# Optimization experiments

Measured on AMD Instinct MI355X. Metric: run time of the kernel, lower is better.

The kernel has to match this reference:

```python
import jax, jax.numpy as jnp
import numpy as np

P = 16384        # nodes per detector layer
NLAYERS = 5      # conf.nlayers (layer labels 0..NLAYERS)
NPROP = 1        # conf.model.nprop
D, S, H = 64, 16, 256   # dyn_features, static_features, deeplayer_nodes
E = 262144       # edges per edge-set (avg degree 16)
NG = 64          # num_graphs


def setup_inputs() -> dict:
    key = jax.random.key(0)
    ks = jax.random.split(key, 20)
    N = P * (NLAYERS + 1)
    F = D + S
    sc = 0.05
    ri = lambda k, shape: jax.random.randint(k, shape, 0, P, dtype=jnp.int32)
    return {
        "x0": jax.random.normal(ks[0], (N, 1), jnp.float32),
        "static": jax.random.normal(ks[1], (N, S), jnp.float32),
        "W1": jax.random.normal(ks[2], (4, F, H), jnp.float32) * sc,
        "b1": jax.random.normal(ks[3], (4, H), jnp.float32) * sc,
        "W2": jax.random.normal(ks[4], (4, H, H), jnp.float32) * sc,
        "b2": jax.random.normal(ks[5], (4, H), jnp.float32) * sc,
        "W3": jax.random.normal(ks[6], (4, H, D), jnp.float32) * sc,
        "b3": jax.random.normal(ks[7], (4, D), jnp.float32) * sc,
        "eps": jnp.zeros((3,), jnp.float32),
        "lin_w": jax.random.normal(ks[8], (D, 1), jnp.float32) * sc,
        "lin_b": jax.random.normal(ks[9], (1,), jnp.float32) * sc,
        "inner_src": ri(ks[10], (NLAYERS, E)),
        "inner_dst": ri(ks[11], (NLAYERS, E)),
        "fwd_src": ri(ks[12], (NLAYERS - 1, E)),
        "fwd_dst": ri(ks[13], (NLAYERS - 1, E)),
        "bwd_src": ri(ks[14], (NLAYERS - 1, E)),
        "bwd_dst": ri(ks[15], (NLAYERS - 1, E)),
        "batch_idx": jax.random.randint(ks[16], (N,), 0, NG, dtype=jnp.int32),
        "num_graphs": NG,
    }


def reference(x0, static, W1, b1, W2, b2, W3, b3, eps, lin_w, lin_b,
              inner_src, inner_dst, fwd_src, fwd_dst, bwd_src, bwd_dst,
              batch_idx, num_graphs):
    N = x0.shape[0]

    def mlp(i, h):
        # dnn(): Linear(F,H)+ReLU, Linear(H,H)+ReLU, Linear(H,D)+ReLU
        h = jax.nn.relu(h @ W1[i] + b1[i])
        h = jax.nn.relu(h @ W2[i] + b2[i])
        return jax.nn.relu(h @ W3[i] + b3[i])

    def gin(i, xs, src, dst):
        # GINConv(train_eps=True): mlp((1+eps)*x + sum_{j in N(v)} x_j)
        aggr = jax.ops.segment_sum(xs[src], dst, num_segments=xs.shape[0])
        return mlp(i, (1.0 + eps[i]) * xs + aggr)

    # x = hstack(batch.x, zeros(N, D-1))
    x = jnp.concatenate([x0, jnp.zeros((N, D - 1), x0.dtype)], axis=1)

    for _ in range(NPROP):
        for il in range(NLAYERS):
            s0 = il * P
            # inner conv on layer il (addstatic over that layer's nodes)
            xs = jnp.concatenate([x[s0:s0 + P], static[s0:s0 + P]], axis=1)
            x = x.at[s0:s0 + P].set(gin(0, xs, inner_src[il], inner_dst[il]))
            if il == NLAYERS - 1:
                continue
            # forward conv over layers il (local [0,P)) and il+1 (local [P,2P))
            xs2 = jnp.concatenate([x[s0:s0 + 2 * P], static[s0:s0 + 2 * P]], axis=1)
            out = gin(1, xs2, fwd_src[il], fwd_dst[il] + P)
            x = x.at[s0 + P:s0 + 2 * P].set(out[P:])
            # node_dnn on target layer
            xt = jnp.concatenate([x[s0 + P:s0 + 2 * P], static[s0 + P:s0 + 2 * P]], axis=1)
            x = x.at[s0 + P:s0 + 2 * P].set(mlp(3, xt))
        for il in range(NLAYERS - 1, 0, -1):
            s0 = (il - 1) * P
            # backward conv: layer il (local [P,2P)) -> layer il-1 (local [0,P))
            xs2 = jnp.concatenate([x[s0:s0 + 2 * P], static[s0:s0 + 2 * P]], axis=1)
            out = gin(2, xs2, bwd_src[il - 1] + P, bwd_dst[il - 1])
            x = x.at[s0:s0 + P].set(out[:P])
            # inner conv on layer il-1
            xs = jnp.concatenate([x[s0:s0 + P], static[s0:s0 + P]], axis=1)
            x = x.at[s0:s0 + P].set(gin(0, xs, inner_src[il - 1], inner_dst[il - 1]))
            # node_dnn on layer il-1
            xt = jnp.concatenate([x[s0:s0 + P], static[s0:s0 + P]], axis=1)
            x = x.at[s0:s0 + P].set(mlp(3, xt))

    pooled = jax.ops.segment_sum(x, batch_idx, num_segments=num_graphs)
    return jax.nn.relu(pooled @ lin_w + lin_b)
```

## Files before the change

kernel.cpp:

```cpp
#include <hip/hip_runtime.h>

#define P 16384
#define NLAYERS 5
#define NND 98304
#define D 64
#define S 16
#define F 80
#define KP1 96
#define H 256
#define EDG 262144
#define NG 64
#define NSETS 13
#define RSP 16385
#define LDP 40
#define LH2 264
#define LXS 100

typedef __attribute__((ext_vector_type(8))) _Float16 f16x8;
typedef __attribute__((ext_vector_type(4))) _Float16 f16x4;
typedef __attribute__((ext_vector_type(4))) float f32x4;

__device__ __forceinline__ void fatomic_add(float* p, float v) {
    unsafeAtomicAdd(p, v);
}

__global__ void k_init_x(const float* __restrict__ x0, float* __restrict__ X,
                         _Float16* __restrict__ Xh,
                         int* __restrict__ deg, float* __restrict__ PL) {
    int idx = blockIdx.x * blockDim.x + threadIdx.x;
    if (idx < NND * D) {
        int row = idx >> 6, f = idx & 63;
        float v = (f == 0) ? x0[row] : 0.0f;
        X[idx] = v;
        Xh[idx] = (_Float16)v;
        return;
    }
    int r = idx - NND * D;
    if (r < NSETS * P) { deg[r] = 0; return; }
    r -= NSETS * P;
    if (r < NG * D) PL[r] = 0.0f;
}

__global__ void k_wconv_all(const float* __restrict__ W1, const float* __restrict__ W2,
                            const float* __restrict__ W3, const float* __restrict__ stat,
                            _Float16* __restrict__ w1, _Float16* __restrict__ w2,
                            _Float16* __restrict__ w3, _Float16* __restrict__ st16) {
    const int n1 = 4 * H * KP1, n2 = 4 * H * H, n3 = 4 * D * H;
    int idx = blockIdx.x * blockDim.x + threadIdx.x;
    if (idx >= n1 + n2 + n3) {
        int i = idx - (n1 + n2 + n3);
        if (i < NND * S) st16[i] = (_Float16)stat[i];
        return;
    }
    const float* W; _Float16* h; int K, N, Kp, i;
    if (idx < n1)              { W = W1; h = w1; K = F; N = H; Kp = KP1; i = idx; }
    else if (idx < n1 + n2)    { W = W2; h = w2; K = H; N = H; Kp = H;   i = idx - n1; }
    else                       { W = W3; h = w3; K = H; N = D; Kp = H;  i = idx - n1 - n2; }
    int set = i / (N * Kp), rem = i - set * (N * Kp);
    int n = rem / Kp, kp = rem - n * Kp;
    float v = (kp < K) ? W[(size_t)set * K * N + (size_t)kp * N + n] : 0.0f;
    h[i] = (_Float16)v;
}

__device__ __forceinline__ const int* set_ptr(int t, const int* inner, const int* fwd,
                                              const int* bwd) {
    if (t < 5) return inner + (size_t)t * EDG;
    if (t < 9) return fwd + (size_t)(t - 5) * EDG;
    return bwd + (size_t)(t - 9) * EDG;
}

__global__ void k_csr_hist(const int* __restrict__ inner_dst, const int* __restrict__ fwd_dst,
                           const int* __restrict__ bwd_dst, int* __restrict__ deg,
                           int* __restrict__ rank) {
    int idx = blockIdx.x * blockDim.x + threadIdx.x;
    if (idx >= NSETS * EDG) return;
    int t = idx >> 18, e = idx & (EDG - 1);
    const int* dstp = set_ptr(t, inner_dst, fwd_dst, bwd_dst);
    rank[idx] = atomicAdd(&deg[t * P + dstp[e]], 1);
}

__global__ __launch_bounds__(1024) void k_csr_scan(const int* __restrict__ deg,
                                                   int* __restrict__ rowstart) {
    __shared__ int part[1024];
    int t = blockIdx.x;
    const int* d = deg + t * P;
    int* rs = rowstart + (size_t)t * RSP;
    int tid = threadIdx.x;
    int base = tid * 16;
    int loc[16], sum = 0;
#pragma unroll
    for (int i = 0; i < 16; ++i) { loc[i] = sum; sum += d[base + i]; }
    part[tid] = sum;
    __syncthreads();
    for (int off = 1; off < 1024; off <<= 1) {
        int v = (tid >= off) ? part[tid - off] : 0;
        __syncthreads();
        part[tid] += v;
        __syncthreads();
    }
    int pre = tid ? part[tid - 1] : 0;
#pragma unroll
    for (int i = 0; i < 16; ++i) rs[base + i] = pre + loc[i];
    if (tid == 1023) rs[P] = pre + sum;
}

__global__ void k_csr_scatter(const int* __restrict__ inner_src, const int* __restrict__ inner_dst,
                              const int* __restrict__ fwd_src, const int* __restrict__ fwd_dst,
                              const int* __restrict__ bwd_src, const int* __restrict__ bwd_dst,
                              const int* __restrict__ rowstart, const int* __restrict__ rank,
                              int* __restrict__ elist) {
    int idx = blockIdx.x * blockDim.x + threadIdx.x;
    if (idx >= NSETS * EDG) return;
    int t = idx >> 18, e = idx & (EDG - 1);
    const int* srcp = set_ptr(t, inner_src, fwd_src, bwd_src);
    const int* dstp = set_ptr(t, inner_dst, fwd_dst, bwd_dst);
    int dv = dstp[e];
    elist[(size_t)t * EDG + rowstart[(size_t)t * RSP + dv] + rank[idx]] = srcp[e];
}

__global__ __launch_bounds__(256) void k_gather_T(const float* __restrict__ X,
                                                  const _Float16* __restrict__ Xh,
                                                  const _Float16* __restrict__ st16,
                                                  const int* __restrict__ elist,
                                                  const int* __restrict__ rowstart,
                                                  _Float16* __restrict__ Th,
                                                  int dst_gbase, int src_gbase,
                                                  const float* __restrict__ eps, int ei,
                                                  const float* __restrict__ stf) {
    int wv = threadIdx.x >> 6, l = threadIdx.x & 63;
    int v = blockIdx.x * 4 + wv;
    int beg = rowstart[v], end = rowstart[v + 1];
    float scale = 1.0f + eps[ei];
    int rg = l >> 4, c = l & 15;
    float ax0 = 0.f, ax1 = 0.f, ax2 = 0.f, ax3 = 0.f, as = 0.f;
    int i = beg;
    for (; i + 4 <= end; i += 4) {
        int s = src_gbase + elist[i + rg];
        f16x4 xv = *(const f16x4*)&Xh[(size_t)s * D + 4 * c];
        ax0 += (float)xv[0]; ax1 += (float)xv[1]; ax2 += (float)xv[2]; ax3 += (float)xv[3];
        as += (float)st16[(size_t)s * S + c];
    }
    if (i < end) {
        int rem = end - i;
        if (rg < rem) {
            int s = src_gbase + elist[i + rg];
            f16x4 xv = *(const f16x4*)&Xh[(size_t)s * D + 4 * c];
            ax0 += (float)xv[0]; ax1 += (float)xv[1]; ax2 += (float)xv[2]; ax3 += (float)xv[3];
            as += (float)st16[(size_t)s * S + c];
        }
    }
#pragma unroll
    for (int off = 16; off < 64; off <<= 1) {
        ax0 += __shfl_xor(ax0, off, 64);
        ax1 += __shfl_xor(ax1, off, 64);
        ax2 += __shfl_xor(ax2, off, 64);
        ax3 += __shfl_xor(ax3, off, 64);
        as  += __shfl_xor(as,  off, 64);
    }
    if (l < 16) {
        int g = dst_gbase + v;
        float4 sx = *(const float4*)&X[(size_t)g * D + 4 * l];
        f16x4 hv;
        hv[0] = (_Float16)(ax0 + scale * sx.x);
        hv[1] = (_Float16)(ax1 + scale * sx.y);
        hv[2] = (_Float16)(ax2 + scale * sx.z);
        hv[3] = (_Float16)(ax3 + scale * sx.w);
        *(f16x4*)&Th[(size_t)v * KP1 + 4 * l] = hv;
        Th[(size_t)v * KP1 + D + l] = (_Float16)(as + scale * stf[(size_t)g * S + l]);
        Th[(size_t)v * KP1 + F + l] = (_Float16)0.0f;
    }
}

template<int MODE>
__global__ __launch_bounds__(512, 2) void k_mlp123(
    const _Float16* __restrict__ Tp,
    const _Float16* __restrict__ W1p, const float* __restrict__ b1,
    const _Float16* __restrict__ W2p, const float* __restrict__ b2,
    const _Float16* __restrict__ W3p, const float* __restrict__ b3,
    float* __restrict__ Xout, _Float16* __restrict__ Xhout,
    const _Float16* __restrict__ W1p3, const float* __restrict__ b13,
    _Float16* __restrict__ H1o,
    int st_gbase, const float* __restrict__ stsrc)
{
    __shared__ _Float16 A1h[64][LDP];
    __shared__ _Float16 B1h[256][LDP];
    __shared__ _Float16 H1s[64][LH2];
    __shared__ _Float16 H2hs[64][LH2];
    __shared__ _Float16 Xsh[(MODE == 1) ? 64 : 1][LXS];

    int tid = threadIdx.x;
    int lane = tid & 63, wid = tid >> 6;
    int la = lane & 15, lg = lane >> 4;
    int r0 = blockIdx.x * 64;

    {
        f32x4 acc0[4][2] = {};
        for (int k0 = 0; k0 < KP1; k0 += 32) {
            if (tid < 256) {
                int ar = tid >> 2, aq = (tid & 3) * 8;
                *(f16x8*)&A1h[ar][aq] = *(const f16x8*)&Tp[(size_t)(r0 + ar) * KP1 + k0 + aq];
            }
#pragma unroll
            for (int j = 0; j < 2; ++j) {
                int id = j * 512 + tid;
                int br = id >> 2, bq = (id & 3) * 8;
                *(f16x8*)&B1h[br][bq] = *(const f16x8*)&W1p[(size_t)br * KP1 + k0 + bq];
            }
            __syncthreads();

            int kf = lg * 8;
            f16x8 ah[4], bh[2];
#pragma unroll
            for (int m = 0; m < 4; ++m) ah[m] = *(const f16x8*)&A1h[m * 16 + la][kf];
#pragma unroll
            for (int n = 0; n < 2; ++n) bh[n] = *(const f16x8*)&B1h[wid * 32 + n * 16 + la][kf];
#pragma unroll
            for (int m = 0; m < 4; ++m)
#pragma unroll
                for (int n = 0; n < 2; ++n)
                    acc0[m][n] = __builtin_amdgcn_mfma_f32_16x16x32_f16(ah[m], bh[n], acc0[m][n], 0, 0, 0);
            __syncthreads();
        }
#pragma unroll
        for (int n = 0; n < 2; ++n) {
            int col = wid * 32 + n * 16 + la;
            float bv = b1[col];
#pragma unroll
            for (int m = 0; m < 4; ++m) {
                int row = m * 16 + lg * 4;
#pragma unroll
                for (int r = 0; r < 4; ++r) {
                    H1s[row + r][col] = (_Float16)fmaxf(acc0[m][n][r] + bv, 0.0f);
                }
            }
        }
        __syncthreads();
    }

    f32x4 acc[4][2] = {};
    for (int k0 = 0; k0 < H; k0 += 32) {
#pragma unroll
        for (int j = 0; j < 2; ++j) {
            int id = j * 512 + tid;
            int br = id >> 2, bq = (id & 3) * 8;
            *(f16x8*)&B1h[br][bq] = *(const f16x8*)&W2p[(size_t)br * H + k0 + bq];
        }
        __syncthreads();

        int kf = lg * 8;
        f16x8 ah[4], bh[2];
#pragma unroll
        for (int m = 0; m < 4; ++m) ah[m] = *(const f16x8*)&H1s[m * 16 + la][k0 + kf];
#pragma unroll
        for (int n = 0; n < 2; ++n) bh[n] = *(const f16x8*)&B1h[wid * 32 + n * 16 + la][kf];
#pragma unroll
        for (int m = 0; m < 4; ++m)
#pragma unroll
            for (int n = 0; n < 2; ++n)
                acc[m][n] = __builtin_amdgcn_mfma_f32_16x16x32_f16(ah[m], bh[n], acc[m][n], 0, 0, 0);
        __syncthreads();
    }
#pragma unroll
    for (int n = 0; n < 2; ++n) {
        int col = wid * 32 + n * 16 + la;
        float bv = b2[col];
#pragma unroll
        for (int m = 0; m < 4; ++m) {
            int row = m * 16 + lg * 4;
#pragma unroll
            for (int r = 0; r < 4; ++r) {
                H2hs[row + r][col] = (_Float16)fmaxf(acc[m][n][r] + bv, 0.0f);
            }
        }
    }
    __syncthreads();

    int wm = wid >> 2, wn = wid & 3;
    f32x4 acc2[2] = {};
    {
        for (int k0 = 0; k0 < H; k0 += 32) {
            if (tid < 256) {
                int br = tid >> 2, bq = (tid & 3) * 8;
                *(f16x8*)&B1h[br][bq] = *(const f16x8*)&W3p[(size_t)br * H + k0 + bq];
            }
            __syncthreads();

            int kf = lg * 8;
            f16x8 ah[2], bh;
#pragma unroll
            for (int m = 0; m < 2; ++m) ah[m] = *(const f16x8*)&H2hs[wm * 32 + m * 16 + la][k0 + kf];
            bh = *(const f16x8*)&B1h[wn * 16 + la][kf];
#pragma unroll
            for (int m = 0; m < 2; ++m)
                acc2[m] = __builtin_amdgcn_mfma_f32_16x16x32_f16(ah[m], bh, acc2[m], 0, 0, 0);
            __syncthreads();
        }
    }
    {
        int col = wn * 16 + la;
        float bv = b3[col];
#pragma unroll
        for (int m = 0; m < 2; ++m) {
            int rloc = wm * 32 + m * 16 + lg * 4;
#pragma unroll
            for (int r = 0; r < 4; ++r) {
                float v = fmaxf(acc2[m][r] + bv, 0.0f);
                if (MODE == 0) {
                    size_t o = (size_t)(r0 + rloc + r) * D + col;
                    Xout[o] = v;
                    Xhout[o] = (_Float16)v;
                } else {
                    Xsh[rloc + r][col] = (_Float16)v;
                }
            }
        }
    }

    if (MODE == 1) {
        {
            int row = tid >> 3, c2 = (tid & 7) * 2;
            int g = st_gbase + r0 + row;
            float2 sv = *(const float2*)&stsrc[(size_t)g * S + c2];
            Xsh[row][D + c2] = (_Float16)sv.x;
            Xsh[row][D + c2 + 1] = (_Float16)sv.y;
            Xsh[row][F + c2] = (_Float16)0.0f;
            Xsh[row][F + c2 + 1] = (_Float16)0.0f;
        }
        __syncthreads();

        f32x4 acc4[4][2] = {};
        for (int k0 = 0; k0 < KP1; k0 += 32) {
#pragma unroll
            for (int j = 0; j < 2; ++j) {
                int id = j * 512 + tid;
                int br = id >> 2, bq = (id & 3) * 8;
                *(f16x8*)&B1h[br][bq] = *(const f16x8*)&W1p3[(size_t)br * KP1 + k0 + bq];
            }
            __syncthreads();

            int kf = lg * 8;
            f16x8 ah[4], bh[2];
#pragma unroll
            for (int m = 0; m < 4; ++m) ah[m] = *(const f16x8*)&Xsh[m * 16 + la][k0 + kf];
#pragma unroll
            for (int n = 0; n < 2; ++n) bh[n] = *(const f16x8*)&B1h[wid * 32 + n * 16 + la][kf];
#pragma unroll
            for (int m = 0; m < 4; ++m)
#pragma unroll
                for (int n = 0; n < 2; ++n)
                    acc4[m][n] = __builtin_amdgcn_mfma_f32_16x16x32_f16(ah[m], bh[n], acc4[m][n], 0, 0, 0);
            __syncthreads();
        }
#pragma unroll
        for (int n = 0; n < 2; ++n) {
            int col = wid * 32 + n * 16 + la;
            float bv = b13[col];
#pragma unroll
            for (int m = 0; m < 4; ++m) {
                int row = r0 + m * 16 + lg * 4;
#pragma unroll
                for (int r = 0; r < 4; ++r) {
                    H1o[(size_t)(row + r) * H + col] = (_Float16)fmaxf(acc4[m][n][r] + bv, 0.0f);
                }
            }
        }
    }
}

__global__ __launch_bounds__(512, 4) void k_mlp23(
    const _Float16* __restrict__ H1p,
    const _Float16* __restrict__ W2p, const float* __restrict__ b2,
    const _Float16* __restrict__ W3p, const float* __restrict__ b3,
    float* __restrict__ Xout, _Float16* __restrict__ Xhout)
{
    __shared__ _Float16 A1h[64][LDP];
    __shared__ _Float16 B1h[256][LDP];
    __shared__ _Float16 H2hs[64][LH2];

    int tid = threadIdx.x;
    int lane = tid & 63, wid = tid >> 6;
    int la = lane & 15, lg = lane >> 4;
    int r0 = blockIdx.x * 64;

    f32x4 acc[4][2] = {};
    for (int k0 = 0; k0 < H; k0 += 32) {
        if (tid < 256) {
            int ar = tid >> 2, aq = (tid & 3) * 8;
            *(f16x8*)&A1h[ar][aq] = *(const f16x8*)&H1p[(size_t)(r0 + ar) * H + k0 + aq];
        }
#pragma unroll
        for (int j = 0; j < 2; ++j) {
            int id = j * 512 + tid;
            int br = id >> 2, bq = (id & 3) * 8;
            *(f16x8*)&B1h[br][bq] = *(const f16x8*)&W2p[(size_t)br * H + k0 + bq];
        }
        __syncthreads();

        int kf = lg * 8;
        f16x8 ah[4], bh[2];
#pragma unroll
        for (int m = 0; m < 4; ++m) ah[m] = *(const f16x8*)&A1h[m * 16 + la][kf];
#pragma unroll
        for (int n = 0; n < 2; ++n) bh[n] = *(const f16x8*)&B1h[wid * 32 + n * 16 + la][kf];
#pragma unroll
        for (int m = 0; m < 4; ++m)
#pragma unroll
            for (int n = 0; n < 2; ++n)
                acc[m][n] = __builtin_amdgcn_mfma_f32_16x16x32_f16(ah[m], bh[n], acc[m][n], 0, 0, 0);
        __syncthreads();
    }
#pragma unroll
    for (int n = 0; n < 2; ++n) {
        int col = wid * 32 + n * 16 + la;
        float bv = b2[col];
#pragma unroll
        for (int m = 0; m < 4; ++m) {
            int row = m * 16 + lg * 4;
#pragma unroll
            for (int r = 0; r < 4; ++r) {
                H2hs[row + r][col] = (_Float16)fmaxf(acc[m][n][r] + bv, 0.0f);
            }
        }
    }
    __syncthreads();

    int wm = wid >> 2, wn = wid & 3;
    f32x4 acc2[2] = {};
    for (int k0 = 0; k0 < H; k0 += 32) {
        if (tid < 256) {
            int br = tid >> 2, bq = (tid & 3) * 8;
            *(f16x8*)&B1h[br][bq] = *(const f16x8*)&W3p[(size_t)br * H + k0 + bq];
        }
        __syncthreads();

        int kf = lg * 8;
        f16x8 ah[2], bh;
#pragma unroll
        for (int m = 0; m < 2; ++m) ah[m] = *(const f16x8*)&H2hs[wm * 32 + m * 16 + la][k0 + kf];
        bh = *(const f16x8*)&B1h[wn * 16 + la][kf];
#pragma unroll
        for (int m = 0; m < 2; ++m)
            acc2[m] = __builtin_amdgcn_mfma_f32_16x16x32_f16(ah[m], bh, acc2[m], 0, 0, 0);
        __syncthreads();
    }
    {
        int col = wn * 16 + la;
        float bv = b3[col];
#pragma unroll
        for (int m = 0; m < 2; ++m) {
            int rloc = wm * 32 + m * 16 + lg * 4;
#pragma unroll
            for (int r = 0; r < 4; ++r) {
                float v = fmaxf(acc2[m][r] + bv, 0.0f);
                size_t o = (size_t)(r0 + rloc + r) * D + col;
                Xout[o] = v;
                Xhout[o] = (_Float16)v;
            }
        }
    }
}

#define PROWS 1024
__global__ __launch_bounds__(256) void k_pool2(const float* __restrict__ X,
                                               const int* __restrict__ bidx,
                                               float* __restrict__ PL) {
    __shared__ float lds[NG * D];
    int tid = threadIdx.x;
    for (int i = tid; i < NG * D; i += 256) lds[i] = 0.0f;
    __syncthreads();
    int base = blockIdx.x * PROWS;
    int f = tid & 63, rg = tid >> 6;
    for (int r = base + rg; r < base + PROWS; r += 4) {
        int g = bidx[r];
        atomicAdd(&lds[g * D + f], X[(size_t)r * D + f]);
    }
    __syncthreads();
    for (int i = tid; i < NG * D; i += 256) {
        float v = lds[i];
        if (v != 0.0f) fatomic_add(&PL[i], v);
    }
}

__global__ void k_final(const float* __restrict__ pooled, const float* __restrict__ lin_w,
                        const float* __restrict__ lin_b, float* __restrict__ out) {
    int g = threadIdx.x;
    if (g >= NG) return;
    float acc = lin_b[0];
#pragma unroll
    for (int d2 = 0; d2 < D; ++d2) acc += pooled[g * D + d2] * lin_w[d2];
    out[g] = fmaxf(acc, 0.0f);
}

extern "C" void kernel_launch(void* const* d_in, const int* in_sizes, int n_in,
                              void* d_out, int out_size, void* d_ws, size_t ws_size,
                              hipStream_t stream) {
    const float* x0    = (const float*)d_in[0];
    const float* stat  = (const float*)d_in[1];
    const float* W1    = (const float*)d_in[2];
    const float* b1    = (const float*)d_in[3];
    const float* W2    = (const float*)d_in[4];
    const float* b2    = (const float*)d_in[5];
    const float* W3    = (const float*)d_in[6];
    const float* b3    = (const float*)d_in[7];
    const float* eps   = (const float*)d_in[8];
    const float* lin_w = (const float*)d_in[9];
    const float* lin_b = (const float*)d_in[10];
    const int* inner_src = (const int*)d_in[11];
    const int* inner_dst = (const int*)d_in[12];
    const int* fwd_src   = (const int*)d_in[13];
    const int* fwd_dst   = (const int*)d_in[14];
    const int* bwd_src   = (const int*)d_in[15];
    const int* bwd_dst   = (const int*)d_in[16];
    const int* bidx      = (const int*)d_in[17];

    float* X  = (float*)d_ws;
    float* PL = X + (size_t)NND * D;
    _Float16* Xh  = (_Float16*)(PL + NG * D);
    _Float16* st16 = Xh + (size_t)NND * D;
    _Float16* Th  = st16 + (size_t)NND * S;
    _Float16* H1p = Th + (size_t)P * KP1;
    _Float16* w1p = H1p + (size_t)P * H;
    _Float16* w2p = w1p + (size_t)4 * H * KP1;
    _Float16* w3p = w2p + (size_t)4 * H * H;
    int* deg      = (int*)(w3p + (size_t)4 * D * H);
    int* rowstart = deg + (size_t)NSETS * P;
    int* rank     = rowstart + (size_t)NSETS * RSP;
    int* elist    = rank + (size_t)NSETS * EDG;

    {
        int tot = NND * D + NSETS * P + NG * D;
        k_init_x<<<(tot + 255) / 256, 256, 0, stream>>>(x0, X, Xh, deg, PL);
    }
    {
        int tot = 4 * H * KP1 + 4 * H * H + 4 * D * H + NND * S;
        k_wconv_all<<<(tot + 255) / 256, 256, 0, stream>>>(W1, W2, W3, stat, w1p, w2p, w3p, st16);
    }
    k_csr_hist<<<(NSETS * EDG) / 256, 256, 0, stream>>>(inner_dst, fwd_dst, bwd_dst, deg, rank);
    k_csr_scan<<<NSETS, 1024, 0, stream>>>(deg, rowstart);
    k_csr_scatter<<<(NSETS * EDG) / 256, 256, 0, stream>>>(inner_src, inner_dst, fwd_src, fwd_dst,
                                                           bwd_src, bwd_dst, rowstart, rank, elist);

    _Float16* w13p = w1p + (size_t)3 * H * KP1;
    const float* b13 = b1 + 3 * H;

    auto conv_plain = [&](int set, int gbase_out) {
        k_mlp123<0><<<P / 64, 512, 0, stream>>>(
            Th,
            w1p + (size_t)set * H * KP1, b1 + set * H,
            w2p + (size_t)set * H * H, b2 + set * H,
            w3p + (size_t)set * D * H, b3 + set * D,
            X + (size_t)gbase_out * D, Xh + (size_t)gbase_out * D,
            nullptr, nullptr, nullptr, 0, nullptr);
    };
    auto conv_fused = [&](int set, int gbase_node) {
        k_mlp123<1><<<P / 64, 512, 0, stream>>>(
            Th,
            w1p + (size_t)set * H * KP1, b1 + set * H,
            w2p + (size_t)set * H * H, b2 + set * H,
            w3p + (size_t)set * D * H, b3 + set * D,
            nullptr, nullptr,
            w13p, b13, H1p, gbase_node, stat);
    };
    auto node_dnn = [&](int gbase_out) {
        k_mlp23<<<P / 64, 512, 0, stream>>>(
            H1p,
            w2p + (size_t)3 * H * H, b2 + 3 * H,
            w3p + (size_t)3 * D * H, b3 + 3 * D,
            X + (size_t)gbase_out * D, Xh + (size_t)gbase_out * D);
    };
    auto gather = [&](int t, int dst_gbase, int src_gbase, int ei) {
        k_gather_T<<<P / 4, 256, 0, stream>>>(
            X, Xh, st16, elist + (size_t)t * EDG, rowstart + (size_t)t * RSP,
            Th, dst_gbase, src_gbase, eps, ei, stat);
    };

    for (int il = 0; il < NLAYERS; ++il) {
        int s0 = il * P;
        gather(il, s0, s0, 0);
        conv_plain(0, s0);
        if (il == NLAYERS - 1) continue;
        gather(5 + il, s0 + P, s0, 1);
        conv_fused(1, s0 + P);
        node_dnn(s0 + P);
    }
    for (int il = NLAYERS - 1; il >= 1; --il) {
        int s0 = (il - 1) * P;
        gather(9 + (il - 1), s0, s0 + P, 2);
        conv_plain(2, s0);
        gather(il - 1, s0, s0, 0);
        conv_fused(0, s0);
        node_dnn(s0);
    }

    k_pool2<<<NND / PROWS, 256, 0, stream>>>(X, bidx, PL);
    k_final<<<1, 64, 0, stream>>>(PL, lin_w, lin_b, (float*)d_out);
}
```

Baseline: 908.7 us.

## Stream layer-2 output through double-buffered LDS slices to cut shared memory

Removes the full 64x256 H2 shared buffer and the separate Xsh buffer. Each warp's layer-2 accumulators are written into a small double-buffered 64x32 slice, interleaved with the layer-3 K loop, and H1s is reused for the mode-1 staging. The launch bound rises from 2 to 4 blocks per SM so the smaller LDS footprint can allow more resident blocks. The cost is that each slice is produced by a single warp, so the epilogue is serialized across eight sync steps, and register pressure may rise under the tighter occupancy bound.

```diff
diff --git a/kernel.cpp b/kernel.cpp
--- a/kernel.cpp
+++ b/kernel.cpp
@@ -14,7 +14,6 @@
 #define RSP 16385
 #define LDP 40
 #define LH2 264
-#define LXS 100
 
 typedef __attribute__((ext_vector_type(8))) _Float16 f16x8;
 typedef __attribute__((ext_vector_type(4))) _Float16 f16x4;
@@ -172,7 +171,7 @@
 }
 
 template<int MODE>
-__global__ __launch_bounds__(512, 2) void k_mlp123(
+__global__ __launch_bounds__(512, 4) void k_mlp123(
     const _Float16* __restrict__ Tp,
     const _Float16* __restrict__ W1p, const float* __restrict__ b1,
     const _Float16* __restrict__ W2p, const float* __restrict__ b2,
@@ -185,8 +184,7 @@
     __shared__ _Float16 A1h[64][LDP];
     __shared__ _Float16 B1h[256][LDP];
     __shared__ _Float16 H1s[64][LH2];
-    __shared__ _Float16 H2hs[64][LH2];
-    __shared__ _Float16 Xsh[(MODE == 1) ? 64 : 1][LXS];
+    __shared__ _Float16 Hb[2][64][LDP];
 
     int tid = threadIdx.x;
     int lane = tid & 63, wid = tid >> 6;
@@ -260,41 +258,41 @@
                 acc[m][n] = __builtin_amdgcn_mfma_f32_16x16x32_f16(ah[m], bh[n], acc[m][n], 0, 0, 0);
         __syncthreads();
     }
-#pragma unroll
-    for (int n = 0; n < 2; ++n) {
-        int col = wid * 32 + n * 16 + la;
-        float bv = b2[col];
-#pragma unroll
-        for (int m = 0; m < 4; ++m) {
-            int row = m * 16 + lg * 4;
-#pragma unroll
-            for (int r = 0; r < 4; ++r) {
-                H2hs[row + r][col] = (_Float16)fmaxf(acc[m][n][r] + bv, 0.0f);
-            }
-        }
-    }
-    __syncthreads();
 
     int wm = wid >> 2, wn = wid & 3;
     f32x4 acc2[2] = {};
-    {
-        for (int k0 = 0; k0 < H; k0 += 32) {
-            if (tid < 256) {
-                int br = tid >> 2, bq = (tid & 3) * 8;
-                *(f16x8*)&B1h[br][bq] = *(const f16x8*)&W3p[(size_t)br * H + k0 + bq];
-            }
-            __syncthreads();
-
-            int kf = lg * 8;
-            f16x8 ah[2], bh;
-#pragma unroll
-            for (int m = 0; m < 2; ++m) ah[m] = *(const f16x8*)&H2hs[wm * 32 + m * 16 + la][k0 + kf];
-            bh = *(const f16x8*)&B1h[wn * 16 + la][kf];
-#pragma unroll
-            for (int m = 0; m < 2; ++m)
-                acc2[m] = __builtin_amdgcn_mfma_f32_16x16x32_f16(ah[m], bh, acc2[m], 0, 0, 0);
-            __syncthreads();
-        }
+    for (int j = 0; j < 8; ++j) {
+        int k0 = j * 32;
+        if (tid < 256) {
+            int br = tid >> 2, bq = (tid & 3) * 8;
+            *(f16x8*)&B1h[br][bq] = *(const f16x8*)&W3p[(size_t)br * H + k0 + bq];
+        }
+        if (wid == j) {
+#pragma unroll
+            for (int n = 0; n < 2; ++n) {
+                int col = n * 16 + la;
+                float bv = b2[k0 + col];
+#pragma unroll
+                for (int m = 0; m < 4; ++m) {
+                    int row = m * 16 + lg * 4;
+#pragma unroll
+                    for (int r = 0; r < 4; ++r) {
+                        Hb[j & 1][row + r][col] = (_Float16)fmaxf(acc[m][n][r] + bv, 0.0f);
+                    }
+                }
+            }
+        }
+        __syncthreads();
+
+        int kf = lg * 8;
+        f16x8 ah[2], bh;
+#pragma unroll
+        for (int m = 0; m < 2; ++m) ah[m] = *(const f16x8*)&Hb[j & 1][wm * 32 + m * 16 + la][kf];
+        bh = *(const f16x8*)&B1h[wn * 16 + la][kf];
+#pragma unroll
+        for (int m = 0; m < 2; ++m)
+            acc2[m] = __builtin_amdgcn_mfma_f32_16x16x32_f16(ah[m], bh, acc2[m], 0, 0, 0);
+        __syncthreads();
     }
     {
         int col = wn * 16 + la;
@@ -310,7 +308,7 @@
                     Xout[o] = v;
                     Xhout[o] = (_Float16)v;
                 } else {
-                    Xsh[rloc + r][col] = (_Float16)v;
+                    H1s[rloc + r][col] = (_Float16)v;
                 }
             }
         }
@@ -321,10 +319,10 @@
             int row = tid >> 3, c2 = (tid & 7) * 2;
             int g = st_gbase + r0 + row;
             float2 sv = *(const float2*)&stsrc[(size_t)g * S + c2];
-            Xsh[row][D + c2] = (_Float16)sv.x;
-            Xsh[row][D + c2 + 1] = (_Float16)sv.y;
-            Xsh[row][F + c2] = (_Float16)0.0f;
-            Xsh[row][F + c2 + 1] = (_Float16)0.0f;
+            H1s[row][D + c2] = (_Float16)sv.x;
+            H1s[row][D + c2 + 1] = (_Float16)sv.y;
+            H1s[row][F + c2] = (_Float16)0.0f;
+            H1s[row][F + c2 + 1] = (_Float16)0.0f;
         }
         __syncthreads();
 
@@ -341,7 +339,7 @@
             int kf = lg * 8;
             f16x8 ah[4], bh[2];
 #pragma unroll
-            for (int m = 0; m < 4; ++m) ah[m] = *(const f16x8*)&Xsh[m * 16 + la][k0 + kf];
+            for (int m = 0; m < 4; ++m) ah[m] = *(const f16x8*)&H1s[m * 16 + la][k0 + kf];
 #pragma unroll
             for (int n = 0; n < 2; ++n) bh[n] = *(const f16x8*)&B1h[wid * 32 + n * 16 + la][kf];
 #pragma unroll
```

After: 955.0 us. 5.1% more time.
